# Performance work log

Measured on AMD Instinct MI355X. Metric: run time of the kernel, lower is better.

The kernel has to match this reference:

```python
import jax, jax.numpy as jnp
import numpy as np

D = H = W = 128  # voxel grid resolution (shape = [1,1,128,128,128] in source)
N = 2_000_000    # number of points


def splat(vals, pts, d, h, w):
    """Adjoint of trilinear F.grid_sample (align_corners=False, zeros padding).
    vals: [N] point values; pts: [N,3] normalized (x,y,z) coords in [-1,1].
    Returns [d,h,w] voxel grid with trilinear scatter-add of vals.
    """
    # unnormalize: pixel = ((coord+1)*size - 1) / 2  (align_corners=False)
    x = ((pts[:, 0] + 1.0) * w - 1.0) * 0.5
    y = ((pts[:, 1] + 1.0) * h - 1.0) * 0.5
    z = ((pts[:, 2] + 1.0) * d - 1.0) * 0.5
    x0 = jnp.floor(x); y0 = jnp.floor(y); z0 = jnp.floor(z)
    fx = x - x0; fy = y - y0; fz = z - z0
    x0i = x0.astype(jnp.int32); y0i = y0.astype(jnp.int32); z0i = z0.astype(jnp.int32)
    grid = jnp.zeros((d * h * w,), dtype=vals.dtype)
    for dz in (0, 1):
        wz = fz if dz else (1.0 - fz)
        for dy in (0, 1):
            wy = fy if dy else (1.0 - fy)
            for dx in (0, 1):
                wx = fx if dx else (1.0 - fx)
                xi = x0i + dx; yi = y0i + dy; zi = z0i + dz
                valid = (xi >= 0) & (xi < w) & (yi >= 0) & (yi < h) & (zi >= 0) & (zi < d)
                idx = jnp.where(valid, (zi * h + yi) * w + xi, 0)
                contrib = jnp.where(valid, wx * wy * wz * vals, 0.0)
                grid = grid.at[idx].add(contrib)
    return grid.reshape(d, h, w)


def huber_sum(pred, gt, delta=1.0):
    diff = pred - gt
    a = jnp.abs(diff)
    return jnp.sum(jnp.where(a <= delta, 0.5 * diff * diff, delta * (a - 0.5 * delta)))


def setup_inputs() -> dict:
    key = jax.random.key(0)
    k1, k2, k3 = jax.random.split(key, 3)
    coords = jax.random.uniform(k1, (1, N, 3), jnp.float32, -0.95, 0.95)
    registration_pred = 0.02 * jax.random.normal(k2, (1, N, 3), jnp.float32)
    registration_gt = 0.02 * jax.random.normal(k3, (1, N, 3), jnp.float32)
    return {"registration_pred": registration_pred,
            "registration_gt": registration_gt,
            "coords": coords}


def reference(registration_pred, registration_gt, coords):
    pred_pts = (coords + registration_pred).reshape(-1, 3)   # [N,3]
    gt_pts = (coords + registration_gt).reshape(-1, 3)       # [N,3]
    vals = jnp.ones((pred_pts.shape[0],), dtype=coords.dtype)
    pred_rast = splat(vals, pred_pts, D, H, W)   # [128,128,128]
    gt_rast = splat(vals, gt_pts, D, H, W)       # [128,128,128]
    return huber_sum(pred_rast, gt_rast)
```

## Files before the change

### kernel.cpp

```cpp
#include <hip/hip_runtime.h>
#include <stdint.h>

constexpr int GRID_R = 128;
constexpr int NVOX = GRID_R * GRID_R * GRID_R;

constexpr int TILE = 16;
constexpr int TPD = GRID_R / TILE;
constexpr int NBINS = TPD * TPD * TPD;
constexpr int CAP = 12288;
constexpr int CUR_STRIDE = 16;
constexpr size_t CUR_BYTES = (size_t)NBINS * CUR_STRIDE * sizeof(uint32_t);
constexpr size_t ITEMS_BYTES = (size_t)NBINS * CAP * sizeof(uint2);
constexpr size_t SORT_WS_NEEDED = CUR_BYTES + ITEMS_BYTES;

constexpr int OB = 9;
constexpr int OARR = OB * OB * OB;
constexpr float Q8 = 16.0f;

__device__ __forceinline__ int axis_tiles(int c0, int* ts, int* ls) {
    int n = 0;
    if ((unsigned)c0 < (unsigned)GRID_R) {
        int tx = c0 >> 4; ts[0] = tx; ls[0] = c0 - (tx << 4); n = 1;
    }
    int c1 = c0 + 1;
    if ((unsigned)c1 < (unsigned)GRID_R) {
        int tx = c1 >> 4;
        if (!n || tx != ts[0]) { ts[n] = tx; ls[n] = c0 - (tx << 4); ++n; }
    }
    return n;
}

template <typename F>
__device__ __forceinline__ void for_each_replica(float px, float py, float pz,
                                                 uint32_t g, F&& emit) {
    float x0f = floorf(px), y0f = floorf(py), z0f = floorf(pz);
    int x0 = (int)x0f, y0 = (int)y0f, z0 = (int)z0f;
    float fx = px - x0f, fy = py - y0f, fz = pz - z0f;

    int txs[2], lxs[2], tys[2], lys[2], tzs[2], lzs[2];
    int ntx = axis_tiles(x0, txs, lxs);
    int nty = axis_tiles(y0, tys, lys);
    int ntz = axis_tiles(z0, tzs, lzs);
    if (!ntx || !nty || !ntz) return;

    uint32_t ufx = (uint32_t)(fx * 65535.0f + 0.5f);
    uint32_t ufy = (uint32_t)(fy * 65535.0f + 0.5f);
    uint32_t ufz = (uint32_t)(fz * 65535.0f + 0.5f);
    uint32_t w0 = ufx | (ufy << 16);

    for (int c = 0; c < ntz; ++c)
        for (int b = 0; b < nty; ++b)
            for (int a = 0; a < ntx; ++a) {
                int bin = (tzs[c] * TPD + tys[b]) * TPD + txs[a];
                uint32_t w1 = ufz |
                              ((uint32_t)(lxs[a] + 1) << 16) |
                              ((uint32_t)(lys[b] + 1) << 21) |
                              ((uint32_t)(lzs[c] + 1) << 26) |
                              (g << 31);
                emit(bin, w0, w1);
            }
}

#define SBLOCK 256
#define PPT 8

__global__ __launch_bounds__(256) void scatter_kernel(
        const float* __restrict__ pred_reg, const float* __restrict__ gt_reg,
        const float* __restrict__ coords, uint32_t* __restrict__ cursors,
        uint2* __restrict__ items, int n) {
    __shared__ uint32_t h[NBINS];
    __shared__ uint32_t base[NBINS];
    int t = threadIdx.x;
    for (int b = t; b < NBINS; b += SBLOCK) h[b] = 0;
    __syncthreads();

    float pa[PPT][3], pb[PPT][3];
    int idxs[PPT];

#pragma unroll
    for (int k = 0; k < PPT; ++k) {
        int i = blockIdx.x * (SBLOCK * PPT) + k * SBLOCK + t;
        idxs[k] = i;
        if (i >= n) continue;
        float cx = coords[3 * i + 0], cy = coords[3 * i + 1], cz = coords[3 * i + 2];
        pa[k][0] = (cx + pred_reg[3 * i + 0] + 1.0f) * 64.0f - 0.5f;
        pa[k][1] = (cy + pred_reg[3 * i + 1] + 1.0f) * 64.0f - 0.5f;
        pa[k][2] = (cz + pred_reg[3 * i + 2] + 1.0f) * 64.0f - 0.5f;
        pb[k][0] = (cx + gt_reg[3 * i + 0] + 1.0f) * 64.0f - 0.5f;
        pb[k][1] = (cy + gt_reg[3 * i + 1] + 1.0f) * 64.0f - 0.5f;
        pb[k][2] = (cz + gt_reg[3 * i + 2] + 1.0f) * 64.0f - 0.5f;
        auto cnt = [&](int bin, uint32_t, uint32_t) { atomicAdd(&h[bin], 1u); };
        for_each_replica(pa[k][0], pa[k][1], pa[k][2], 0u, cnt);
        for_each_replica(pb[k][0], pb[k][1], pb[k][2], 1u, cnt);
    }
    __syncthreads();

    for (int b = t; b < NBINS; b += SBLOCK) {
        uint32_t c = h[b];
        base[b] = c ? atomicAdd(&cursors[b * CUR_STRIDE], c) : 0u;
        h[b] = 0;
    }
    __syncthreads();

#pragma unroll
    for (int k = 0; k < PPT; ++k) {
        if (idxs[k] >= n) continue;
        auto put = [&](int bin, uint32_t w0, uint32_t w1) {
            uint32_t r = atomicAdd(&h[bin], 1u);
            uint32_t s = base[bin] + r;
            if (s < (uint32_t)CAP)
                items[(size_t)bin * CAP + s] = make_uint2(w0, w1);
        };
        for_each_replica(pa[k][0], pa[k][1], pa[k][2], 0u, put);
        for_each_replica(pb[k][0], pb[k][1], pb[k][2], 1u, put);
    }
}

#define ABLOCK 1024

__device__ __forceinline__ void accum_item8(uint64_t* __restrict__ U,
                                            uint32_t wx, uint32_t wy) {
    float fx = (float)(wx & 0xffffu) * (1.0f / 65535.0f);
    float fy = (float)(wx >> 16) * (1.0f / 65535.0f);
    float fz = (float)(wy & 0xffffu) * (1.0f / 65535.0f);
    int lx1 = (int)((wy >> 16) & 31u);
    int ly1 = (int)((wy >> 21) & 31u);
    int lz1 = (int)((wy >> 26) & 31u);
    uint32_t g = wy >> 31;

    int px = lx1 & 1, xb = lx1 >> 1;
    int py = ly1 & 1, yb = ly1 >> 1;
    int pz = lz1 & 1, zb = lz1 >> 1;
    uint64_t* arr = U + ((g << 3) | (pz << 2) | (py << 1) | px) * OARR;
    int idx = (zb * OB + yb) * OB + xb;

    float wx1 = fx, wx0 = 1.0f - fx;
    float wy1 = fy, wy0 = 1.0f - fy;
    float wz1 = fz, wz0 = 1.0f - fz;
    float w00 = wx0 * wy0 * Q8, w10 = wx1 * wy0 * Q8;
    float w01 = wx0 * wy1 * Q8, w11 = wx1 * wy1 * Q8;

    uint32_t lo = (uint32_t)(w00 * wz0 + 0.5f) |
                  ((uint32_t)(w10 * wz0 + 0.5f) << 8) |
                  ((uint32_t)(w01 * wz0 + 0.5f) << 16) |
                  ((uint32_t)(w11 * wz0 + 0.5f) << 24);
    uint32_t hi = (uint32_t)(w00 * wz1 + 0.5f) |
                  ((uint32_t)(w10 * wz1 + 0.5f) << 8) |
                  ((uint32_t)(w01 * wz1 + 0.5f) << 16) |
                  ((uint32_t)(w11 * wz1 + 0.5f) << 24);
    atomicAdd((unsigned long long*)&arr[idx],
              (unsigned long long)((uint64_t)lo | ((uint64_t)hi << 32)));
}

__global__ __launch_bounds__(ABLOCK, 4) void accum_kernel(
        const uint2* __restrict__ items, const uint32_t* __restrict__ cursors,
        float* __restrict__ out) {
    __shared__ uint64_t U[16 * OARR];
    __shared__ float wsum[ABLOCK / 64];
    int bin = blockIdx.x, t = threadIdx.x;

    for (int j = t; j < 16 * OARR; j += ABLOCK) U[j] = 0ull;
    __syncthreads();

    uint32_t cnt = cursors[bin * CUR_STRIDE];
    if (cnt > (uint32_t)CAP) cnt = CAP;
    const uint2* seg = items + (size_t)bin * CAP;
    const uint4* seg4 = (const uint4*)seg;
    uint32_t npair = cnt >> 1;

    uint32_t i = t;
    uint4 w = (i < npair) ? seg4[i] : make_uint4(0, 0, 0, 0);
    while (i < npair) {
        uint32_t inext = i + ABLOCK;
        uint4 wn = (inext < npair) ? seg4[inext] : make_uint4(0, 0, 0, 0);
        accum_item8(U, w.x, w.y);
        accum_item8(U, w.z, w.w);
        w = wn; i = inext;
    }
    if ((cnt & 1) && t == 0) {
        uint2 lw = seg[cnt - 1];
        accum_item8(U, lw.x, lw.y);
    }
    __syncthreads();

    float s = 0.0f;
    for (int j = t; j < TILE * TILE * TILE; j += ABLOCK) {
        int x = (j & 15) + 1, y = ((j >> 4) & 15) + 1, z = (j >> 8) + 1;
        float v[2];
#pragma unroll
        for (int g = 0; g < 2; ++g) {
            uint32_t acc = 0;
#pragma unroll
            for (int pz = 0; pz < 2; ++pz)
#pragma unroll
                for (int py = 0; py < 2; ++py)
#pragma unroll
                    for (int px = 0; px < 2; ++px) {
                        int cx = ((x & 1) == px) ? x : x - 1;  int dx = x - cx;
                        int cy = ((y & 1) == py) ? y : y - 1;  int dy = y - cy;
                        int cz = ((z & 1) == pz) ? z : z - 1;  int dz = z - cz;
                        uint64_t q = U[((g << 3) | (pz << 2) | (py << 1) | px) *
                                           OARR +
                                       ((cz >> 1) * OB + (cy >> 1)) * OB +
                                       (cx >> 1)];
                        acc += (uint32_t)(q >> (((dz << 2) | (dy << 1) | dx)
                                                << 3)) & 0xFFu;
                    }
            v[g] = (float)acc;
        }
        float d = (v[0] - v[1]) * (1.0f / Q8);
        float aa = fabsf(d);
        s += (aa <= 1.0f) ? 0.5f * d * d : (aa - 0.5f);
    }
#pragma unroll
    for (int off = 32; off > 0; off >>= 1) s += __shfl_down(s, off, 64);
    int lane = t & 63, wid = t >> 6;
    if (!lane) wsum[wid] = s;
    __syncthreads();
    if (!t) {
        float tot = 0.0f;
#pragma unroll
        for (int wv = 0; wv < ABLOCK / 64; ++wv) tot += wsum[wv];
        unsafeAtomicAdd(out, tot);
    }
}

__device__ __forceinline__ void splat_point(float nx, float ny, float nz,
                                            float* __restrict__ grid) {
    float x = (nx + 1.0f) * 64.0f - 0.5f;
    float y = (ny + 1.0f) * 64.0f - 0.5f;
    float z = (nz + 1.0f) * 64.0f - 0.5f;
    float x0f = floorf(x), y0f = floorf(y), z0f = floorf(z);
    float fx = x - x0f, fy = y - y0f, fz = z - z0f;
    int x0 = (int)x0f, y0 = (int)y0f, z0 = (int)z0f;
    int xs[2] = {x0, x0 + 1}, ys[2] = {y0, y0 + 1}, zs[2] = {z0, z0 + 1};
    float wxs[2] = {1.0f - fx, fx}, wys[2] = {1.0f - fy, fy}, wzs[2] = {1.0f - fz, fz};
#pragma unroll
    for (int dz = 0; dz < 2; ++dz) {
        int zi = zs[dz]; if ((unsigned)zi >= (unsigned)GRID_R) continue;
#pragma unroll
        for (int dy = 0; dy < 2; ++dy) {
            int yi = ys[dy]; if ((unsigned)yi >= (unsigned)GRID_R) continue;
            float wzy = wzs[dz] * wys[dy];
            int basei = (zi * GRID_R + yi) * GRID_R;
#pragma unroll
            for (int dx = 0; dx < 2; ++dx) {
                int xi = xs[dx]; if ((unsigned)xi >= (unsigned)GRID_R) continue;
                unsafeAtomicAdd(&grid[basei + xi], wzy * wxs[dx]);
            }
        }
    }
}

__global__ void splat_kernel(const float* __restrict__ pred_reg,
                             const float* __restrict__ gt_reg,
                             const float* __restrict__ coords,
                             float* __restrict__ gridA, float* __restrict__ gridB,
                             int n) {
    int i = blockIdx.x * blockDim.x + threadIdx.x;
    if (i >= n) return;
    float cx = coords[3 * i + 0], cy = coords[3 * i + 1], cz = coords[3 * i + 2];
    splat_point(cx + pred_reg[3 * i + 0], cy + pred_reg[3 * i + 1],
                cz + pred_reg[3 * i + 2], gridA);
    splat_point(cx + gt_reg[3 * i + 0], cy + gt_reg[3 * i + 1],
                cz + gt_reg[3 * i + 2], gridB);
}

__global__ void huber_kernel(const float4* __restrict__ A,
                             const float4* __restrict__ B,
                             float* __restrict__ out) {
    int i = blockIdx.x * blockDim.x + threadIdx.x;
    float4 a = A[i], b = B[i];
    auto h1 = [](float d) { float x = fabsf(d);
                            return (x <= 1.0f) ? 0.5f * d * d : (x - 0.5f); };
    float s = h1(a.x - b.x) + h1(a.y - b.y) + h1(a.z - b.z) + h1(a.w - b.w);
#pragma unroll
    for (int off = 32; off > 0; off >>= 1) s += __shfl_down(s, off, 64);
    __shared__ float wsum[4];
    int lane = threadIdx.x & 63, wid = threadIdx.x >> 6;
    if (!lane) wsum[wid] = s;
    __syncthreads();
    if (!threadIdx.x) atomicAdd(out, wsum[0] + wsum[1] + wsum[2] + wsum[3]);
}

extern "C" void kernel_launch(void* const* d_in, const int* in_sizes, int n_in,
                              void* d_out, int out_size, void* d_ws, size_t ws_size,
                              hipStream_t stream) {
    const float* pred_reg = (const float*)d_in[0];
    const float* gt_reg   = (const float*)d_in[1];
    const float* coords   = (const float*)d_in[2];
    float* outp = (float*)d_out;
    int n = in_sizes[2] / 3;

    hipMemsetAsync(d_out, 0, sizeof(float), stream);

    if (ws_size >= SORT_WS_NEEDED) {
        uint32_t* cursors = (uint32_t*)d_ws;
        uint2* items = (uint2*)((char*)d_ws + CUR_BYTES);
        hipMemsetAsync(cursors, 0, CUR_BYTES, stream);

        int sblocks = (n + SBLOCK * PPT - 1) / (SBLOCK * PPT);
        scatter_kernel<<<sblocks, SBLOCK, 0, stream>>>(pred_reg, gt_reg, coords,
                                                       cursors, items, n);
        accum_kernel<<<NBINS, ABLOCK, 0, stream>>>(items, cursors, outp);
    } else {
        float* gridA = (float*)d_ws;
        float* gridB = gridA + NVOX;
        hipMemsetAsync(d_ws, 0, (size_t)2 * NVOX * sizeof(float), stream);
        int blocks = (n + 255) / 256;
        splat_kernel<<<blocks, 256, 0, stream>>>(pred_reg, gt_reg, coords,
                                                 gridA, gridB, n);
        huber_kernel<<<NVOX / 4 / 256, 256, 0, stream>>>((const float4*)gridA,
                                                         (const float4*)gridB, outp);
    }
}
```

Baseline: 193.0 us.

## Replace global cursor binning with per-block fixed slots plus overflow list

The scatter kernel now does a single pass. Each block writes items into fixed per-(bin, block) slots of capacity BCAP and records a per-block count, which removes the count pass, the global cursor atomics and the second replay of points. Items beyond BCAP go to a global overflow list through a global atomic. The accumulate kernel scans every slot, including empty ones, and also scans the whole overflow list in every bin block. Block size goes up to 1024, and slots over capacity in the overflow list are dropped, which risks wasted reads and, if overflow is large, lost items.

```diff
diff --git a/kernel.cpp b/kernel.cpp
--- a/kernel.cpp
+++ b/kernel.cpp
@@ -7,11 +7,9 @@
 constexpr int TILE = 16;
 constexpr int TPD = GRID_R / TILE;
 constexpr int NBINS = TPD * TPD * TPD;
-constexpr int CAP = 12288;
-constexpr int CUR_STRIDE = 16;
-constexpr size_t CUR_BYTES = (size_t)NBINS * CUR_STRIDE * sizeof(uint32_t);
-constexpr size_t ITEMS_BYTES = (size_t)NBINS * CAP * sizeof(uint2);
-constexpr size_t SORT_WS_NEEDED = CUR_BYTES + ITEMS_BYTES;
+constexpr int BCAP = 48;
+constexpr int OVF_CAP = 65536;
+constexpr int MAXNBLK = 512;
 
 constexpr int OB = 9;
 constexpr int OARR = OB * OB * OB;
@@ -61,59 +59,51 @@
             }
 }
 
-#define SBLOCK 256
+#define SBLOCK 1024
 #define PPT 8
 
-__global__ __launch_bounds__(256) void scatter_kernel(
+__global__ __launch_bounds__(SBLOCK) void scatter_kernel(
         const float* __restrict__ pred_reg, const float* __restrict__ gt_reg,
-        const float* __restrict__ coords, uint32_t* __restrict__ cursors,
-        uint2* __restrict__ items, int n) {
+        const float* __restrict__ coords, uint32_t* __restrict__ counts,
+        uint32_t* __restrict__ ovf_cnt, uint4* __restrict__ ovf,
+        uint2* __restrict__ items, int n, int nblk) {
     __shared__ uint32_t h[NBINS];
-    __shared__ uint32_t base[NBINS];
-    int t = threadIdx.x;
+    int t = threadIdx.x, blk = blockIdx.x;
     for (int b = t; b < NBINS; b += SBLOCK) h[b] = 0;
     __syncthreads();
 
-    float pa[PPT][3], pb[PPT][3];
-    int idxs[PPT];
+    const int binstride = nblk * BCAP;
+    const int blkbase = blk * BCAP;
+
+    auto put = [&](int bin, uint32_t w0, uint32_t w1) {
+        uint32_t slot = atomicAdd(&h[bin], 1u);
+        if (slot < (uint32_t)BCAP) {
+            items[(size_t)bin * binstride + blkbase + slot] = make_uint2(w0, w1);
+        } else {
+            uint32_t o = atomicAdd(ovf_cnt, 1u);
+            if (o < (uint32_t)OVF_CAP)
+                ovf[o] = make_uint4((uint32_t)bin, w0, w1, 0u);
+        }
+    };
 
 #pragma unroll
     for (int k = 0; k < PPT; ++k) {
-        int i = blockIdx.x * (SBLOCK * PPT) + k * SBLOCK + t;
-        idxs[k] = i;
+        int i = blk * (SBLOCK * PPT) + k * SBLOCK + t;
         if (i >= n) continue;
         float cx = coords[3 * i + 0], cy = coords[3 * i + 1], cz = coords[3 * i + 2];
-        pa[k][0] = (cx + pred_reg[3 * i + 0] + 1.0f) * 64.0f - 0.5f;
-        pa[k][1] = (cy + pred_reg[3 * i + 1] + 1.0f) * 64.0f - 0.5f;
-        pa[k][2] = (cz + pred_reg[3 * i + 2] + 1.0f) * 64.0f - 0.5f;
-        pb[k][0] = (cx + gt_reg[3 * i + 0] + 1.0f) * 64.0f - 0.5f;
-        pb[k][1] = (cy + gt_reg[3 * i + 1] + 1.0f) * 64.0f - 0.5f;
-        pb[k][2] = (cz + gt_reg[3 * i + 2] + 1.0f) * 64.0f - 0.5f;
-        auto cnt = [&](int bin, uint32_t, uint32_t) { atomicAdd(&h[bin], 1u); };
-        for_each_replica(pa[k][0], pa[k][1], pa[k][2], 0u, cnt);
-        for_each_replica(pb[k][0], pb[k][1], pb[k][2], 1u, cnt);
-    }
-    __syncthreads();
-
-    for (int b = t; b < NBINS; b += SBLOCK) {
-        uint32_t c = h[b];
-        base[b] = c ? atomicAdd(&cursors[b * CUR_STRIDE], c) : 0u;
-        h[b] = 0;
-    }
-    __syncthreads();
-
-#pragma unroll
-    for (int k = 0; k < PPT; ++k) {
-        if (idxs[k] >= n) continue;
-        auto put = [&](int bin, uint32_t w0, uint32_t w1) {
-            uint32_t r = atomicAdd(&h[bin], 1u);
-            uint32_t s = base[bin] + r;
-            if (s < (uint32_t)CAP)
-                items[(size_t)bin * CAP + s] = make_uint2(w0, w1);
-        };
-        for_each_replica(pa[k][0], pa[k][1], pa[k][2], 0u, put);
-        for_each_replica(pb[k][0], pb[k][1], pb[k][2], 1u, put);
-    }
+        float ax = (cx + pred_reg[3 * i + 0] + 1.0f) * 64.0f - 0.5f;
+        float ay = (cy + pred_reg[3 * i + 1] + 1.0f) * 64.0f - 0.5f;
+        float az = (cz + pred_reg[3 * i + 2] + 1.0f) * 64.0f - 0.5f;
+        float bx = (cx + gt_reg[3 * i + 0] + 1.0f) * 64.0f - 0.5f;
+        float by = (cy + gt_reg[3 * i + 1] + 1.0f) * 64.0f - 0.5f;
+        float bz = (cz + gt_reg[3 * i + 2] + 1.0f) * 64.0f - 0.5f;
+        for_each_replica(ax, ay, az, 0u, put);
+        for_each_replica(bx, by, bz, 1u, put);
+    }
+    __syncthreads();
+
+    for (int b = t; b < NBINS; b += SBLOCK)
+        counts[blk * NBINS + b] = min(h[b], (uint32_t)BCAP);
 }
 
 #define ABLOCK 1024
@@ -153,33 +143,35 @@
 }
 
 __global__ __launch_bounds__(ABLOCK, 4) void accum_kernel(
-        const uint2* __restrict__ items, const uint32_t* __restrict__ cursors,
-        float* __restrict__ out) {
+        const uint2* __restrict__ items, const uint32_t* __restrict__ counts,
+        const uint32_t* __restrict__ ovf_cnt, const uint4* __restrict__ ovf,
+        float* __restrict__ out, int nblk) {
     __shared__ uint64_t U[16 * OARR];
+    __shared__ uint32_t cL[MAXNBLK];
     __shared__ float wsum[ABLOCK / 64];
     int bin = blockIdx.x, t = threadIdx.x;
 
     for (int j = t; j < 16 * OARR; j += ABLOCK) U[j] = 0ull;
-    __syncthreads();
-
-    uint32_t cnt = cursors[bin * CUR_STRIDE];
-    if (cnt > (uint32_t)CAP) cnt = CAP;
-    const uint2* seg = items + (size_t)bin * CAP;
-    const uint4* seg4 = (const uint4*)seg;
-    uint32_t npair = cnt >> 1;
-
-    uint32_t i = t;
-    uint4 w = (i < npair) ? seg4[i] : make_uint4(0, 0, 0, 0);
-    while (i < npair) {
-        uint32_t inext = i + ABLOCK;
-        uint4 wn = (inext < npair) ? seg4[inext] : make_uint4(0, 0, 0, 0);
-        accum_item8(U, w.x, w.y);
-        accum_item8(U, w.z, w.w);
-        w = wn; i = inext;
-    }
-    if ((cnt & 1) && t == 0) {
-        uint2 lw = seg[cnt - 1];
-        accum_item8(U, lw.x, lw.y);
+    for (int j = t; j < nblk; j += ABLOCK) cL[j] = counts[j * NBINS + bin];
+    __syncthreads();
+
+    const int slots = nblk * BCAP;
+    const uint2* seg = items + (size_t)bin * slots;
+
+    for (int idx = t; idx < slots; idx += ABLOCK) {
+        int blk = idx / BCAP;
+        int slot = idx - blk * BCAP;
+        if ((uint32_t)slot < cL[blk]) {
+            uint2 w = seg[idx];
+            accum_item8(U, w.x, w.y);
+        }
+    }
+
+    uint32_t novf = *ovf_cnt;
+    if (novf > (uint32_t)OVF_CAP) novf = OVF_CAP;
+    for (uint32_t j = t; j < novf; j += ABLOCK) {
+        uint4 e = ovf[j];
+        if (e.x == (uint32_t)bin) accum_item8(U, e.y, e.z);
     }
     __syncthreads();
 
@@ -294,15 +286,29 @@
 
     hipMemsetAsync(d_out, 0, sizeof(float), stream);
 
-    if (ws_size >= SORT_WS_NEEDED) {
-        uint32_t* cursors = (uint32_t*)d_ws;
-        uint2* items = (uint2*)((char*)d_ws + CUR_BYTES);
-        hipMemsetAsync(cursors, 0, CUR_BYTES, stream);
-
-        int sblocks = (n + SBLOCK * PPT - 1) / (SBLOCK * PPT);
-        scatter_kernel<<<sblocks, SBLOCK, 0, stream>>>(pred_reg, gt_reg, coords,
-                                                       cursors, items, n);
-        accum_kernel<<<NBINS, ABLOCK, 0, stream>>>(items, cursors, outp);
+    int nblk = (n + SBLOCK * PPT - 1) / (SBLOCK * PPT);
+
+    size_t counts_b = (size_t)NBINS * nblk * sizeof(uint32_t);
+    size_t counts_off = 0;
+    size_t ovfcnt_off = (counts_off + counts_b + 15) & ~(size_t)15;
+    size_t ovf_off = ovfcnt_off + 16;
+    size_t items_off = (ovf_off + (size_t)OVF_CAP * sizeof(uint4) + 15) & ~(size_t)15;
+    size_t items_b = (size_t)NBINS * nblk * BCAP * sizeof(uint2);
+    size_t total = items_off + items_b;
+
+    if (nblk <= MAXNBLK && ws_size >= total) {
+        uint32_t* counts = (uint32_t*)((char*)d_ws + counts_off);
+        uint32_t* ovf_cnt = (uint32_t*)((char*)d_ws + ovfcnt_off);
+        uint4* ovf = (uint4*)((char*)d_ws + ovf_off);
+        uint2* items = (uint2*)((char*)d_ws + items_off);
+
+        hipMemsetAsync(ovf_cnt, 0, 16, stream);
+
+        scatter_kernel<<<nblk, SBLOCK, 0, stream>>>(pred_reg, gt_reg, coords,
+                                                    counts, ovf_cnt, ovf,
+                                                    items, n, nblk);
+        accum_kernel<<<NBINS, ABLOCK, 0, stream>>>(items, counts, ovf_cnt,
+                                                   ovf, outp, nblk);
     } else {
         float* gridA = (float*)d_ws;
         float* gridB = gridA + NVOX;
```

After: 599.8 us. 3.11x slower.
